# Kernel tuning notes

Measured on AMD Instinct MI355X. Metric: run time of the kernel, lower is better.

Reference implementation:

```python
import jax, jax.numpy as jnp
import numpy as np


def setup_inputs() -> dict:
    key = jax.random.key(0)
    kq, kk, kv = jax.random.split(key, 3)
    B, H, S, D = 1, 16, 4096, 64
    q = jax.random.normal(kq, (B, H, S, D), dtype=jnp.float32)
    k = jax.random.normal(kk, (B, H, S, D), dtype=jnp.float32)
    v = jax.random.normal(kv, (B, H, S, D), dtype=jnp.float32)
    return {"q": q, "k": k, "v": v}


def reference(q, k, v):
    # softmax(q @ k^T * d^-0.5 + causal_bias) @ v
    S = q.shape[-2]
    scale = q.shape[-1] ** -0.5
    logits = jnp.einsum("bhqd,bhkd->bhqk", q, k) * scale  # [B,H,S,S]
    causal = jnp.tril(jnp.ones((S, S), dtype=bool))  # additive bias: 0 allowed, -inf future
    logits = jnp.where(causal, logits, -jnp.inf)
    probs = jax.nn.softmax(logits, axis=-1)
    return jnp.einsum("bhqk,bhkd->bhqd", probs, v)
```

## Files before the change

### kernel.cpp

```cpp
#include <hip/hip_runtime.h>
#include <hip/hip_bf16.h>
#include <math.h>

typedef __attribute__((ext_vector_type(8))) short short8;
typedef __attribute__((ext_vector_type(4))) short short4v;
typedef __attribute__((ext_vector_type(4))) float f32x4;
typedef __attribute__((ext_vector_type(4))) unsigned uint4v;
typedef __attribute__((ext_vector_type(2))) unsigned uint2v;

#if __has_builtin(__builtin_amdgcn_permlane32_swap) && __has_builtin(__builtin_amdgcn_permlane16_swap)
#define HAVE_PLSWAP 1
#else
#define HAVE_PLSWAP 0
#endif

#define S_LEN 4096
#define D_DIM 64
#define QBLK 64
#define NHEAD 16
#define QSCALE (0.125f * 1.44269504088896340736f)
#define NEG_BIG (-3.0e38f)
#define DEFER_THR 8.0f

__device__ __forceinline__ short f2bf(float f) {
  union { float f; unsigned u; } x;
  x.f = f;
  unsigned r = x.u + 0x7FFFu + ((x.u >> 16) & 1u);
  return (short)(r >> 16);
}

__device__ __forceinline__ unsigned cvtpk_bf16(float lo, float hi) {
  unsigned r;
  asm("v_cvt_pk_bf16_f32 %0, %1, %2" : "=v"(r) : "v"(lo), "v"(hi));
  return r;
}

__device__ __forceinline__ float f3max(float a, float b, float c) {
  return fmaxf(fmaxf(a, b), c);
}

__device__ __forceinline__ void gload_lds16(const void* g, void* l) {
  __builtin_amdgcn_global_load_lds(
      (const __attribute__((address_space(1))) unsigned*)g,
      (__attribute__((address_space(3))) unsigned*)l, 16, 0, 0);
}

__global__ __launch_bounds__(256) void conv_kv(
    const float* __restrict__ K, const float* __restrict__ V,
    short* __restrict__ Kb, short* __restrict__ Vt) {
  const int h = blockIdx.y;
  const int s0 = blockIdx.x * 64;
  const int tid = threadIdx.x;
  __shared__ short vt[64][68];
  const float* kp = K + ((size_t)h * S_LEN + s0) * D_DIM;
  const float* vp = V + ((size_t)h * S_LEN + s0) * D_DIM;
  short* kb = Kb + ((size_t)h * S_LEN + s0) * D_DIM;
#pragma unroll
  for (int p = 0; p < 4; ++p) {
    const int idx = tid + (p << 8);
    const int row = idx >> 4, c4 = (idx & 15) << 2;
    const float4 kf = *(const float4*)(kp + row * D_DIM + c4);
    short4v ks;
    ks[0] = f2bf(kf.x); ks[1] = f2bf(kf.y); ks[2] = f2bf(kf.z); ks[3] = f2bf(kf.w);
    *(short4v*)(kb + row * D_DIM + c4) = ks;
    const float4 vf = *(const float4*)(vp + row * D_DIM + c4);
    short4v vs;
    vs[0] = f2bf(vf.x); vs[1] = f2bf(vf.y); vs[2] = f2bf(vf.z); vs[3] = f2bf(vf.w);
    *(short4v*)&vt[row][c4] = vs;
  }
  __syncthreads();
  short* vo = Vt + ((size_t)h * D_DIM) * S_LEN + s0;
#pragma unroll
  for (int p = 0; p < 4; ++p) {
    const int idx = tid + (p << 8);
    const int d = idx >> 4, sc = (idx & 15) << 2;
    short4v x;
    x[0] = vt[sc + 0][d]; x[1] = vt[sc + 1][d];
    x[2] = vt[sc + 2][d]; x[3] = vt[sc + 3][d];
    *(short4v*)(vo + (size_t)d * S_LEN + sc) = x;
  }
}

__global__ __launch_bounds__(512, 4) void attn_fwd(
    const float* __restrict__ Q, const short* __restrict__ Kb,
    const short* __restrict__ Vt, float* __restrict__ O) {
  const int lid = blockIdx.x;
  const int xcd = lid & 7, slot = lid >> 3;
  const int h = xcd * 2 + (slot & 1);
  const int pr = slot >> 1;

  const int tid = threadIdx.x;
  const int w = tid >> 6;
  const int grp = w >> 2;
  const int wq = w & 3;
  const int l = tid & 63, g = l >> 4, c = l & 15;

#if HAVE_PLSWAP
  __shared__ __align__(16) char SMEM[65536];
#else
  __shared__ __align__(16) char SMEM[81920];
  short* P0 = (short*)(SMEM + 65536);
#endif
  short* Kg = (short*)SMEM + grp * 8192;
  short* Vg = (short*)(SMEM + 32768) + grp * 8192;

  const float* Qh = Q + ((size_t)h * S_LEN) * D_DIM;
  const char* Kh = (const char*)(Kb + ((size_t)h * S_LEN) * D_DIM);
  const char* Vh = (const char*)(Vt + ((size_t)h * D_DIM) * S_LEN);
  float* Oh = O + ((size_t)h * S_LEN) * D_DIM;

  auto stage = [&](int tg, int b) {
    const char* kg = Kh + (size_t)(64 * tg) * 128;
    const char* vg = Vh + 128 * tg;
#pragma unroll
    for (int i = 0; i < 2; ++i) {
      const int qr = wq * 2 + i;
      const int r = qr * 8 + (l >> 3);
      const int ch = l & 7;
      const int swz = (ch ^ (r & 7)) << 4;
      gload_lds16(kg + (size_t)r * 128 + swz, Kg + b * 4096 + qr * 512);
      gload_lds16(vg + (size_t)r * (S_LEN * 2) + swz, Vg + b * 4096 + qr * 512);
    }
  };

  for (int rep = 0; rep < 2; ++rep) {
    const int a = rep ? (63 - pr) : pr;
    const int qb0 = a * QBLK;
    const int q0 = qb0 + wq * 16;
    const int qg = q0 + c;
    const int nmax = (a >> 1) + 1;
    const int nloc = (a >= grp) ? (((a - grp) >> 1) + 1) : 0;

    if (rep) __syncthreads();
    if (nloc > 0) stage(grp, 0);

    short8 qf[2];
    {
      const float* qp = Qh + (size_t)qg * D_DIM;
#pragma unroll
      for (int hh = 0; hh < 2; ++hh) {
        short8 aa;
#pragma unroll
        for (int j = 0; j < 8; ++j) aa[j] = f2bf(qp[hh * 32 + g * 8 + j] * QSCALE);
        qf[hh] = aa;
      }
    }

    f32x4 o[4];
#pragma unroll
    for (int i = 0; i < 4; ++i) o[i] = (f32x4)0.f;
    float m_r = 0.f, l_r = 0.f;

    short8 vfp[8];
    short8 pfp[2];
    bool pend = false;

    __syncthreads();
    int cur = 0;

    for (int tl = 0; tl < nmax; ++tl) {
      const int tg = 2 * tl + grp;
      if (tl + 1 < nloc) stage(tg + 2, cur ^ 1);
      if (tl < nloc) {
        const short* Kl = Kg + cur * 4096;
        const short* Vl = Vg + cur * 4096;

        const float negm = -m_r;
        f32x4 s[4];
        __builtin_amdgcn_s_setprio(1);
#pragma unroll
        for (int sub = 0; sub < 4; ++sub) {
          const int kvr = sub * 16 + c;
          f32x4 acc = (f32x4)negm;
#pragma unroll
          for (int hh = 0; hh < 2; ++hh) {
            const int idx = (kvr * 64 + hh * 32 + g * 8) ^ ((c & 7) << 3);
            acc = __builtin_amdgcn_mfma_f32_16x16x32_bf16(
                *(const short8*)&Kl[idx], qf[hh], acc, 0, 0, 0);
          }
          s[sub] = acc;
        }
        if (pend) {
#pragma unroll
          for (int dt = 0; dt < 4; ++dt)
#pragma unroll
            for (int hk = 0; hk < 2; ++hk)
              o[dt] = __builtin_amdgcn_mfma_f32_16x16x32_bf16(
                  vfp[dt * 2 + hk], pfp[hk], o[dt], 0, 0, 0);
        }
        __builtin_amdgcn_s_setprio(0);

#pragma unroll
        for (int dt = 0; dt < 4; ++dt)
#pragma unroll
          for (int hk = 0; hk < 2; ++hk) {
            const int dr = dt * 16 + c;
            const int idx = (dr * 64 + hk * 32 + g * 8) ^ ((c & 7) << 3);
            vfp[dt * 2 + hk] = *(const short8*)&Vl[idx];
          }

        if (64 * tg + 63 > q0) {
          const int thr = qg - 64 * tg - 4 * g;
#pragma unroll
          for (int sub = 0; sub < 4; ++sub)
#pragma unroll
            for (int r = 0; r < 4; ++r)
              if (16 * sub + r > thr) s[sub][r] = NEG_BIG;
        }

        float t0 = f3max(s[0][0], s[0][1], s[0][2]);
        float t1 = f3max(s[0][3], s[1][0], s[1][1]);
        float t2 = f3max(s[1][2], s[1][3], s[2][0]);
        float t3 = f3max(s[2][1], s[2][2], s[2][3]);
        float t4 = f3max(s[3][0], s[3][1], s[3][2]);
        float pm = fmaxf(f3max(t0, t1, t2), f3max(t3, t4, s[3][3]));
        pm = fmaxf(pm, __shfl_xor(pm, 16));
        pm = fmaxf(pm, __shfl_xor(pm, 32));
        if (__any(pm > DEFER_THR)) {
          const float d = fmaxf(pm, 0.f);
          const float al = __builtin_amdgcn_exp2f(-d);
          m_r += d;
          l_r *= al;
#pragma unroll
          for (int dt = 0; dt < 4; ++dt)
#pragma unroll
            for (int r = 0; r < 4; ++r) o[dt][r] *= al;
#pragma unroll
          for (int sub = 0; sub < 4; ++sub)
#pragma unroll
            for (int r = 0; r < 4; ++r) s[sub][r] -= d;
        }
        float rs = 0.f;
#pragma unroll
        for (int sub = 0; sub < 4; ++sub)
#pragma unroll
          for (int r = 0; r < 4; ++r) {
            s[sub][r] = __builtin_amdgcn_exp2f(s[sub][r]);
            rs += s[sub][r];
          }
        l_r += rs;

#if HAVE_PLSWAP
        {
          unsigned u0[4], u1[4];
#pragma unroll
          for (int sub = 0; sub < 4; ++sub) {
            u0[sub] = cvtpk_bf16(s[sub][0], s[sub][1]);
            u1[sub] = cvtpk_bf16(s[sub][2], s[sub][3]);
          }
          uint2v r0 = __builtin_amdgcn_permlane32_swap(u0[0], u0[1], false, false);
          r0 = __builtin_amdgcn_permlane16_swap(r0[0], r0[1], false, false);
          uint2v r1 = __builtin_amdgcn_permlane32_swap(u1[0], u1[1], false, false);
          r1 = __builtin_amdgcn_permlane16_swap(r1[0], r1[1], false, false);
          uint2v r2 = __builtin_amdgcn_permlane32_swap(u0[2], u0[3], false, false);
          r2 = __builtin_amdgcn_permlane16_swap(r2[0], r2[1], false, false);
          uint2v r3 = __builtin_amdgcn_permlane32_swap(u1[2], u1[3], false, false);
          r3 = __builtin_amdgcn_permlane16_swap(r3[0], r3[1], false, false);
          uint4v w0v = {r0[0], r1[0], r0[1], r1[1]};
          uint4v w1v = {r2[0], r3[0], r2[1], r3[1]};
          pfp[0] = __builtin_bit_cast(short8, w0v);
          pfp[1] = __builtin_bit_cast(short8, w1v);
        }
#else
        {
          short* Pw = P0 + w * 1024;
#pragma unroll
          for (int sub = 0; sub < 4; ++sub) {
            const unsigned u0 = cvtpk_bf16(s[sub][0], s[sub][1]);
            const unsigned u1 = cvtpk_bf16(s[sub][2], s[sub][3]);
            const unsigned long long uu = ((unsigned long long)u1 << 32) | u0;
            const int idx = (c * 64 + sub * 16 + g * 4) ^ ((c & 7) << 3);
            *(unsigned long long*)&Pw[idx] = uu;
          }
#pragma unroll
          for (int hk = 0; hk < 2; ++hk) {
            const int idx = (c * 64 + hk * 32 + g * 8) ^ ((c & 7) << 3);
            pfp[hk] = *(const short8*)&Pw[idx];
          }
        }
#endif
        pend = true;
      }

      __syncthreads();
      cur ^= 1;
    }

    if (pend) {
      __builtin_amdgcn_s_setprio(1);
#pragma unroll
      for (int dt = 0; dt < 4; ++dt)
#pragma unroll
        for (int hk = 0; hk < 2; ++hk)
          o[dt] = __builtin_amdgcn_mfma_f32_16x16x32_bf16(
              vfp[dt * 2 + hk], pfp[hk], o[dt], 0, 0, 0);
      __builtin_amdgcn_s_setprio(0);
    }

    float* mrg = (float*)(SMEM + 32768) + wq * 1152;
    if (grp == 1) {
#pragma unroll
      for (int dt = 0; dt < 4; ++dt)
#pragma unroll
        for (int r = 0; r < 4; ++r) mrg[(dt * 4 + r) * 64 + l] = o[dt][r];
      mrg[1024 + l] = l_r;
      mrg[1088 + l] = m_r;
    }
    __syncthreads();
    if (grp == 0) {
      const float m1 = mrg[1088 + l];
      const float l1 = mrg[1024 + l];
      const float M = fmaxf(m_r, m1);
      const float a0 = __builtin_amdgcn_exp2f(m_r - M);
      const float a1 = __builtin_amdgcn_exp2f(m1 - M);
      float lm = l_r * a0 + l1 * a1;
      lm += __shfl_xor(lm, 16);
      lm += __shfl_xor(lm, 32);
      const float inv = 1.f / lm;
      float* scr = (float*)SMEM + wq * (16 * 68);
#pragma unroll
      for (int dt = 0; dt < 4; ++dt)
#pragma unroll
        for (int r = 0; r < 4; ++r) {
          const float om = o[dt][r] * a0 + mrg[(dt * 4 + r) * 64 + l] * a1;
          scr[c * 68 + dt * 16 + g * 4 + r] = om * inv;
        }
      const int q_l = l >> 2, prt = l & 3;
      const float* sr = scr + q_l * 68 + prt * 16;
      float* op = Oh + (size_t)(q0 + q_l) * D_DIM + prt * 16;
#pragma unroll
      for (int k2 = 0; k2 < 4; ++k2)
        *(f32x4*)(op + k2 * 4) = *(const f32x4*)(sr + k2 * 4);
    }
  }
}

extern "C" void kernel_launch(void* const* d_in, const int* in_sizes, int n_in,
                              void* d_out, int out_size, void* d_ws, size_t ws_size,
                              hipStream_t stream) {
  const float* q = (const float*)d_in[0];
  const float* k = (const float*)d_in[1];
  const float* v = (const float*)d_in[2];
  float* out = (float*)d_out;
  short* kb = (short*)d_ws;
  short* vt = kb + (size_t)NHEAD * S_LEN * D_DIM;
  dim3 cgrid(S_LEN / 64, NHEAD);
  conv_kv<<<cgrid, dim3(256), 0, stream>>>(k, v, kb, vt);
  attn_fwd<<<dim3(512), dim3(512), 0, stream>>>(q, kb, vt, out);
}
```

Before: 80.73 us.

## Split K and V staging and read V from LDS at PV time

```diff
diff --git a/kernel.cpp b/kernel.cpp
--- a/kernel.cpp
+++ b/kernel.cpp
@@ -109,9 +109,8 @@
   const char* Vh = (const char*)(Vt + ((size_t)h * D_DIM) * S_LEN);
   float* Oh = O + ((size_t)h * S_LEN) * D_DIM;
 
-  auto stage = [&](int tg, int b) {
+  auto stageK = [&](int tg, int b) {
     const char* kg = Kh + (size_t)(64 * tg) * 128;
-    const char* vg = Vh + 128 * tg;
 #pragma unroll
     for (int i = 0; i < 2; ++i) {
       const int qr = wq * 2 + i;
@@ -119,6 +118,16 @@
       const int ch = l & 7;
       const int swz = (ch ^ (r & 7)) << 4;
       gload_lds16(kg + (size_t)r * 128 + swz, Kg + b * 4096 + qr * 512);
+    }
+  };
+  auto stageV = [&](int tg, int b) {
+    const char* vg = Vh + 128 * tg;
+#pragma unroll
+    for (int i = 0; i < 2; ++i) {
+      const int qr = wq * 2 + i;
+      const int r = qr * 8 + (l >> 3);
+      const int ch = l & 7;
+      const int swz = (ch ^ (r & 7)) << 4;
       gload_lds16(vg + (size_t)r * (S_LEN * 2) + swz, Vg + b * 4096 + qr * 512);
     }
   };
@@ -132,7 +141,7 @@
     const int nloc = (a >= grp) ? (((a - grp) >> 1) + 1) : 0;
 
     if (rep) __syncthreads();
-    if (nloc > 0) stage(grp, 0);
+    if (nloc > 0) stageK(grp, 0);
 
     short8 qf[2];
     {
@@ -151,7 +160,6 @@
     for (int i = 0; i < 4; ++i) o[i] = (f32x4)0.f;
     float m_r = 0.f, l_r = 0.f;
 
-    short8 vfp[8];
     short8 pfp[2];
     bool pend = false;
 
@@ -160,10 +168,11 @@
 
     for (int tl = 0; tl < nmax; ++tl) {
       const int tg = 2 * tl + grp;
-      if (tl + 1 < nloc) stage(tg + 2, cur ^ 1);
+      if (tl + 1 < nloc) stageK(tg + 2, cur ^ 1);
+      if (tl < nloc) stageV(tg, cur ^ 1);
       if (tl < nloc) {
         const short* Kl = Kg + cur * 4096;
-        const short* Vl = Vg + cur * 4096;
+        const short* Vp = Vg + cur * 4096;
 
         const float negm = -m_r;
         f32x4 s[4];
@@ -182,22 +191,17 @@
         }
         if (pend) {
 #pragma unroll
-          for (int dt = 0; dt < 4; ++dt)
-#pragma unroll
-            for (int hk = 0; hk < 2; ++hk)
+          for (int dt = 0; dt < 4; ++dt) {
+            const int dr = dt * 16 + c;
+#pragma unroll
+            for (int hk = 0; hk < 2; ++hk) {
+              const int idx = (dr * 64 + hk * 32 + g * 8) ^ ((c & 7) << 3);
               o[dt] = __builtin_amdgcn_mfma_f32_16x16x32_bf16(
-                  vfp[dt * 2 + hk], pfp[hk], o[dt], 0, 0, 0);
+                  *(const short8*)&Vp[idx], pfp[hk], o[dt], 0, 0, 0);
+            }
+          }
         }
         __builtin_amdgcn_s_setprio(0);
-
-#pragma unroll
-        for (int dt = 0; dt < 4; ++dt)
-#pragma unroll
-          for (int hk = 0; hk < 2; ++hk) {
-            const int dr = dt * 16 + c;
-            const int idx = (dr * 64 + hk * 32 + g * 8) ^ ((c & 7) << 3);
-            vfp[dt * 2 + hk] = *(const short8*)&Vl[idx];
-          }
 
         if (64 * tg + 63 > q0) {
           const int thr = qg - 64 * tg - 4 * g;
@@ -287,15 +291,21 @@
     }
 
     if (pend) {
+      const short* Vp = Vg + (nloc & 1) * 4096;
       __builtin_amdgcn_s_setprio(1);
 #pragma unroll
-      for (int dt = 0; dt < 4; ++dt)
-#pragma unroll
-        for (int hk = 0; hk < 2; ++hk)
+      for (int dt = 0; dt < 4; ++dt) {
+        const int dr = dt * 16 + c;
+#pragma unroll
+        for (int hk = 0; hk < 2; ++hk) {
+          const int idx = (dr * 64 + hk * 32 + g * 8) ^ ((c & 7) << 3);
           o[dt] = __builtin_amdgcn_mfma_f32_16x16x32_bf16(
-              vfp[dt * 2 + hk], pfp[hk], o[dt], 0, 0, 0);
+              *(const short8*)&Vp[idx], pfp[hk], o[dt], 0, 0, 0);
+        }
+      }
       __builtin_amdgcn_s_setprio(0);
     }
+    __syncthreads();
 
     float* mrg = (float*)(SMEM + 32768) + wq * 1152;
     if (grp == 1) {
```

Result: faster. 74.22 us (-8.1%).
